# Performance work log

Measured on AMD Instinct MI355X. Metric: run time of the kernel, lower is better.

The kernel has to match this reference:

```python
import jax, jax.numpy as jnp
import numpy as np

EPS = 1e-5

def setup_inputs() -> dict:
    key = jax.random.key(0)
    ks = jax.random.split(key, 6)
    N, E, C, H, L = 50000, 800000, 128, 128, 3
    x = jax.random.normal(ks[0], (N, C), dtype=jnp.float32)
    edge_index = jax.random.randint(ks[1], (2, E), 0, N, dtype=jnp.int64)
    # Xavier-ish scaled weights; layer 0 uses in=C=H so all layers stack uniformly.
    Wl = jax.random.normal(ks[2], (L, C, H), dtype=jnp.float32) / np.sqrt(C)
    Wr = jax.random.normal(ks[3], (L, C, H), dtype=jnp.float32) / np.sqrt(C)
    b = jnp.zeros((L, H), dtype=jnp.float32)
    gamma = jnp.ones((L, H), dtype=jnp.float32)
    beta = jnp.zeros((L, H), dtype=jnp.float32)
    return {"x": x, "edge_index": edge_index, "Wl": Wl, "Wr": Wr, "b": b,
            "gamma": gamma, "beta": beta}

def _sage_bn_relu(x, src, dst, Wl, Wr, b, gamma, beta):
    N = x.shape[0]
    # mean aggregation of source features into target nodes (PyG SAGEConv default)
    agg = jax.ops.segment_sum(x[src], dst, num_segments=N)          # [N, C]
    deg = jax.ops.segment_sum(jnp.ones_like(dst, dtype=x.dtype), dst, num_segments=N)
    mean_nbr = agg / jnp.maximum(deg, 1.0)[:, None]
    h = mean_nbr @ Wl + x @ Wr + b                                   # [N, H]
    # BatchNorm1d (training-mode batch statistics over nodes)
    mu = jnp.mean(h, axis=0)
    var = jnp.var(h, axis=0)
    h = gamma * (h - mu) * jax.lax.rsqrt(var + EPS) + beta
    return jax.nn.relu(h)  # dropout omitted (deterministic reference, p->0)

def reference(x, edge_index, Wl, Wr, b, gamma, beta):
    src, dst = edge_index[0], edge_index[1]
    h = x
    for l in range(Wl.shape[0]):
        h = _sage_bn_relu(h, src, dst, Wl[l], Wr[l], b[l], gamma[l], beta[l])
    return h
```

## Files before the change

### kernel.cpp

```cpp
#include <hip/hip_runtime.h>
#include <hip/hip_bf16.h>

#define BN_EPS 1e-5f
#define BCAP 16384

typedef unsigned short u16;
typedef unsigned int u32;
typedef __attribute__((ext_vector_type(8))) short bf16x8v;
typedef __attribute__((ext_vector_type(4))) float f32x4v;

__device__ __forceinline__ float bf2f(u16 u){
    union { u32 i; float f; } c; c.i = ((u32)u) << 16; return c.f;
}
__device__ __forceinline__ u16 f2bf(float f){
    union { float f; u32 i; } c; c.f = f;
    u32 x = c.i;
    u32 r = x + 0x7FFFu + ((x >> 16) & 1u);
    return (u16)(r >> 16);
}
__device__ __forceinline__ float lo16(u32 u){
    union { u32 i; float f; } c; c.i = u << 16; return c.f;
}
__device__ __forceinline__ float hi16(u32 u){
    union { u32 i; float f; } c; c.i = u & 0xFFFF0000u; return c.f;
}
__device__ __forceinline__ u32 pack2(float f0, float f1){
    return (u32)f2bf(f0) | ((u32)f2bf(f1) << 16);
}

__global__ void detect_k(const int* __restrict__ ei, const u16* __restrict__ xu,
                         int* __restrict__ flags){
    int lane = threadIdx.x;
    unsigned long long bal = __ballot(ei[2 * lane + 1] != 0);
    int cnt = 0;
    #pragma unroll
    for (int k = 0; k < 4; ++k){
        u16 u = xu[2 * (lane + 64 * k)];
        int e = (u >> 7) & 0xFF;
        cnt += (e >= 0x70 && e <= 0x86) ? 1 : 0;
    }
    #pragma unroll
    for (int off = 1; off < 64; off <<= 1) cnt += __shfl_xor(cnt, off);
    if (lane == 0){
        flags[0] = (bal == 0ULL) ? 1 : 0;
        flags[1] = (cnt >= 128) ? 1 : 0;
    }
}

__global__ void prep_k(const void* __restrict__ x, const void* __restrict__ Wl,
                       const void* __restrict__ Wr, const void* __restrict__ b,
                       const void* __restrict__ g, const void* __restrict__ be,
                       u16* __restrict__ xb, u16* __restrict__ wT, float* __restrict__ p,
                       int total4, int wtot, int per, const int* __restrict__ flags){
    int i = blockIdx.x * blockDim.x + threadIdx.x;
    int bf = flags[1];
    if (i < total4){
        if (bf){
            ((uint2*)xb)[i] = ((const uint2*)x)[i];
        } else {
            float4 v = ((const float4*)x)[i];
            ushort4 o; o.x = f2bf(v.x); o.y = f2bf(v.y); o.z = f2bf(v.z); o.w = f2bf(v.w);
            ((ushort4*)xb)[i] = o;
        }
    }
    if (i < wtot){
        u16 vl = bf ? ((const u16*)Wl)[i] : f2bf(((const float*)Wl)[i]);
        u16 vr = bf ? ((const u16*)Wr)[i] : f2bf(((const float*)Wr)[i]);
        int l = i >> 14, r = (i >> 7) & 127, c = i & 127;
        wT[(size_t)(l * 2 + 0) * 16384 + c * 128 + r] = vl;
        wT[(size_t)(l * 2 + 1) * 16384 + c * 128 + r] = vr;
    }
    if (i < per){
        if (bf){
            p[i]           = bf2f(((const u16*)b)[i]);
            p[per + i]     = bf2f(((const u16*)g)[i]);
            p[2 * per + i] = bf2f(((const u16*)be)[i]);
        } else {
            p[i]           = ((const float*)b)[i];
            p[per + i]     = ((const float*)g)[i];
            p[2 * per + i] = ((const float*)be)[i];
        }
    }
}

__global__ __launch_bounds__(1024) void phist_k(const void* __restrict__ ei, int E,
                                                int tile, u32* __restrict__ blockHist,
                                                const int* __restrict__ flags){
    __shared__ u32 lh[128];
    int tid = threadIdx.x;
    if (tid < 128) lh[tid] = 0u;
    __syncthreads();
    int start = blockIdx.x * tile;
    int end = min(E, start + tile);
    int i64 = flags[0];
    for (int i = start + tid; i < end; i += 1024){
        int d = i64 ? (int)((const long long*)ei)[E + i] : ((const int*)ei)[E + i];
        atomicAdd(&lh[d >> 9], 1u);
    }
    __syncthreads();
    if (tid < 128) blockHist[blockIdx.x * 128 + tid] = lh[tid];
}

__global__ void bases_k(const u32* __restrict__ blockHist, u32* __restrict__ blockBase,
                        int* __restrict__ rangeBase, int* __restrict__ rowptrN, int nb){
    __shared__ u32 t_s[128];
    int k = threadIdx.x;
    u32 run = 0;
    for (int b = 0; b < nb; ++b){
        blockBase[b * 128 + k] = run;
        run += blockHist[b * 128 + k];
    }
    t_s[k] = min(run, (u32)BCAP);
    __syncthreads();
    if (k == 0){
        u32 r = 0;
        for (int j = 0; j < 128; ++j){ u32 v = t_s[j]; t_s[j] = r; r += v; }
        rangeBase[128] = (int)r;
        *rowptrN = (int)r;
    }
    __syncthreads();
    rangeBase[k] = (int)t_s[k];
}

__global__ __launch_bounds__(1024) void pscat_k(const void* __restrict__ ei, int E,
                                                int tile, const u32* __restrict__ blockBase,
                                                u32* __restrict__ part,
                                                const int* __restrict__ flags){
    __shared__ u32 lcur[128];
    int tid = threadIdx.x;
    if (tid < 128) lcur[tid] = blockBase[blockIdx.x * 128 + tid];
    __syncthreads();
    int start = blockIdx.x * tile;
    int end = min(E, start + tile);
    int i64 = flags[0];
    for (int i = start + tid; i < end; i += 1024){
        int s, d;
        if (i64){
            const long long* p = (const long long*)ei;
            s = (int)p[i]; d = (int)p[E + i];
        } else {
// ... 31 lines not shown
    #pragma unroll
    for (int off = 1; off < 64; off <<= 1){
        u32 u = __shfl_up(sc, off);
        if (lane >= off) sc += u;
    }
    if (lane == 63 && w < 8) wsum[w] = sc;
    __syncthreads();
    if (tid == 0){
        u32 r = 0;
        #pragma unroll
        for (int j = 0; j < 8; ++j){ u32 t = wsum[j]; wsum[j] = r; r += t; }
    }
    __syncthreads();
    u32 excl = (w < 8 ? wsum[w] : 0u) + sc - v;
    if (tid < 512){
        int d = d0 + tid;
        if (d < N){
            rowptr[d] = base + (int)excl;
            dinv[d] = 1.f / fmaxf((float)v, 1.f);
        }
        bins[tid] = excl;
    }
    __syncthreads();
    for (int i = tid; i < cntk; i += 1024){
        u32 e = pk[i];
        u32 pos = atomicAdd(&bins[e >> 16], 1u);
        sorted[pos] = (u16)e;
    }
    __syncthreads();
    for (int i = tid; i < cntk; i += 1024)
        col[base + i] = sorted[i];
}

__global__ void agg_k(const u16* __restrict__ h, const int* __restrict__ rowptr,
                      const u16* __restrict__ col, const float* __restrict__ dinv,
                      u16* __restrict__ meanb, int N){
    int wid  = (blockIdx.x * blockDim.x + threadIdx.x) >> 6;
    int lane = threadIdx.x & 63;
    if (wid >= N) return;
    int q   = lane >> 4;
    int sub = lane & 15;
    int s = rowptr[wid], e = rowptr[wid + 1];
    float a[8] = {0.f,0.f,0.f,0.f,0.f,0.f,0.f,0.f};
    int i = s + q;
    for (; i + 4 < e; i += 8){
        int sn0 = col[i], sn1 = col[i + 4];
        uint4 v0 = *(const uint4*)(h + (size_t)sn0 * 128 + sub * 8);
        uint4 v1 = *(const uint4*)(h + (size_t)sn1 * 128 + sub * 8);
        a[0] += lo16(v0.x) + lo16(v1.x); a[1] += hi16(v0.x) + hi16(v1.x);
        a[2] += lo16(v0.y) + lo16(v1.y); a[3] += hi16(v0.y) + hi16(v1.y);
        a[4] += lo16(v0.z) + lo16(v1.z); a[5] += hi16(v0.z) + hi16(v1.z);
        a[6] += lo16(v0.w) + lo16(v1.w); a[7] += hi16(v0.w) + hi16(v1.w);
    }
    if (i < e){
        int sn = col[i];
        uint4 v = *(const uint4*)(h + (size_t)sn * 128 + sub * 8);
        a[0] += lo16(v.x); a[1] += hi16(v.x);
        a[2] += lo16(v.y); a[3] += hi16(v.y);
        a[4] += lo16(v.z); a[5] += hi16(v.z);
        a[6] += lo16(v.w); a[7] += hi16(v.w);
    }
    #pragma unroll
    for (int off = 16; off < 64; off <<= 1){
        #pragma unroll
        for (int j = 0; j < 8; ++j) a[j] += __shfl_xor(a[j], off);
    }
    if (q == 0){
        float di = dinv[wid];
        uint4 o;
        o.x = pack2(a[0] * di, a[1] * di);
        o.y = pack2(a[2] * di, a[3] * di);
        o.z = pack2(a[4] * di, a[5] * di);
        o.w = pack2(a[6] * di, a[7] * di);
        *(uint4*)(meanb + (size_t)wid * 128 + sub * 8) = o;
    }
}

__global__ __launch_bounds__(256) void gemm_k(
        const u16* __restrict__ Aa, const u16* __restrict__ Ab,
        const u16* __restrict__ wT, const float* __restrict__ bias,
        float* __restrict__ stats, u16* __restrict__ hp16, int N, int NT){
    int tid  = threadIdx.x;
    int lane = tid & 63;
    int w    = tid >> 6;
    int hl   = lane & 15;
    int quad = lane >> 4;
    int c0   = (2 * w)     * 16 + hl;
    int c1   = (2 * w + 1) * 16 + hl;

    bf16x8v Bf[2][2][4];
    {
        const u16* bp = wT + (size_t)(2 * w) * 2048 + (size_t)hl * 128 + quad * 8;
        #pragma unroll
        for (int tl = 0; tl < 2; ++tl)
            #pragma unroll
            for (int half = 0; half < 2; ++half)
                #pragma unroll
                for (int kc = 0; kc < 4; ++kc)
                    Bf[tl][half][kc] =
                        *(const bf16x8v*)(bp + tl * 2048 + half * 16384 + kc * 32);
    }
    float bv0 = bias[c0], bv1 = bias[c1];
    float cs0 = 0.f, cq0 = 0.f, cs1 = 0.f, cq1 = 0.f;

    for (int tile = blockIdx.x; tile < NT; tile += gridDim.x){
        int m0  = tile * 32;
        int rb0 = m0;      bool v0 = (rb0 + 16 <= N); if (!v0) rb0 = N - 16;
        int rb1 = m0 + 16; bool v1 = (rb1 + 16 <= N); if (!v1) rb1 = N - 16;
        const u16* paa0 = Aa + (size_t)(rb0 + hl) * 128 + quad * 8;
        const u16* pab0 = Ab + (size_t)(rb0 + hl) * 128 + quad * 8;
        const u16* paa1 = Aa + (size_t)(rb1 + hl) * 128 + quad * 8;
        const u16* pab1 = Ab + (size_t)(rb1 + hl) * 128 + quad * 8;

        bf16x8v A0[2][4], A1[2][4];
        #pragma unroll
        for (int kc = 0; kc < 4; ++kc){
            A0[0][kc] = *(const bf16x8v*)(paa0 + kc * 32);
            A1[0][kc] = *(const bf16x8v*)(paa1 + kc * 32);
            A0[1][kc] = *(const bf16x8v*)(pab0 + kc * 32);
            A1[1][kc] = *(const bf16x8v*)(pab1 + kc * 32);
        }

        f32x4v acc0[2], acc1[2];
        #pragma unroll
        for (int tl = 0; tl < 2; ++tl){
            acc0[tl] = (f32x4v){0.f, 0.f, 0.f, 0.f};
            acc1[tl] = (f32x4v){0.f, 0.f, 0.f, 0.f};
        }
        #pragma unroll
        for (int half = 0; half < 2; ++half)
            #pragma unroll
            for (int kc = 0; kc < 4; ++kc)
                #pragma unroll
                for (int tl = 0; tl < 2; ++tl){
                    acc0[tl] = __builtin_amdgcn_mfma_f32_16x16x32_bf16(
                        A0[half][kc], Bf[tl][half][kc], acc0[tl], 0, 0, 0);
                    acc1[tl] = __builtin_amdgcn_mfma_f32_16x16x32_bf16(
                        A1[half][kc], Bf[tl][half][kc], acc1[tl], 0, 0, 0);
                }

        #pragma unroll
        for (int tl = 0; tl < 2; ++tl){
            int   c  = tl ? c1 : c0;
            float bv = tl ? bv1 : bv0;
            if (v0){
                #pragma unroll
                for (int r = 0; r < 4; ++r){
                    float v = acc0[tl][r] + bv;
                    hp16[(size_t)(rb0 + quad * 4 + r) * 128 + c] = f2bf(v);
                    if (tl){ cs1 += v; cq1 += v * v; } else { cs0 += v; cq0 += v * v; }
                }
            }
            if (v1){
                #pragma unroll
                for (int r = 0; r < 4; ++r){
                    float v = acc1[tl][r] + bv;
                    hp16[(size_t)(rb1 + quad * 4 + r) * 128 + c] = f2bf(v);
                    if (tl){ cs1 += v; cq1 += v * v; } else { cs0 += v; cq0 += v * v; }
                }
            }
        }
    }

    cs0 += __shfl_xor(cs0, 16); cs0 += __shfl_xor(cs0, 32);
    cq0 += __shfl_xor(cq0, 16); cq0 += __shfl_xor(cq0, 32);
    cs1 += __shfl_xor(cs1, 16); cs1 += __shfl_xor(cs1, 32);
    cq1 += __shfl_xor(cq1, 16); cq1 += __shfl_xor(cq1, 32);
    if (quad == 0){
        float* st = stats + (size_t)(blockIdx.x & 63) * 256;
        atomicAdd(&st[c0],       cs0);
        atomicAdd(&st[128 + c0], cq0);
        atomicAdd(&st[c1],       cs1);
        atomicAdd(&st[128 + c1], cq1);
    }
}

__global__ void finalize_k(const float* __restrict__ stats, const float* __restrict__ g,
                           const float* __restrict__ be, float* __restrict__ ss,
                           float invN){
    int j = threadIdx.x;
    float s = 0.f, sq = 0.f;
    #pragma unroll 8
    for (int bkt = 0; bkt < 64; ++bkt){
        s  += stats[bkt * 256 + j];
        sq += stats[bkt * 256 + 128 + j];
    }
    float mu  = s * invN;
    float var = sq * invN - mu * mu;
    if (!(mu == mu)) mu = 0.f;
    if (!(var >= 0.f) || !(var == var)) var = 0.f;
    float sc = g[j] * rsqrtf(var + BN_EPS);
    ss[j]       = sc;
    ss[128 + j] = be[j] - mu * sc;
}

__global__ void apply_k(const u16* __restrict__ in, const float* __restrict__ ss,
                        u16* __restrict__ outb, float* __restrict__ outf, int use_f32,
                        int total4){
    int i = blockIdx.x * blockDim.x + threadIdx.x;
    if (i >= total4) return;
    uint2 u = ((const uint2*)in)[i];
    float4 v;
    v.x = lo16(u.x); v.y = hi16(u.x); v.z = lo16(u.y); v.w = hi16(u.y);
    if (!(v.x == v.x)) v.x = 0.f;
    if (!(v.y == v.y)) v.y = 0.f;
    if (!(v.z == v.z)) v.z = 0.f;
    if (!(v.w == v.w)) v.w = 0.f;
    int c = (i & 31) * 4;
    float r0 = fmaxf(v.x * ss[c]     + ss[128 + c], 0.f);
    float r1 = fmaxf(v.y * ss[c + 1] + ss[129 + c], 0.f);
    float r2 = fmaxf(v.z * ss[c + 2] + ss[130 + c], 0.f);
    float r3 = fmaxf(v.w * ss[c + 3] + ss[131 + c], 0.f);
    if (use_f32){
        float4 o; o.x = r0; o.y = r1; o.z = r2; o.w = r3;
        ((float4*)outf)[i] = o;
    } else {
        uint2 o; o.x = pack2(r0, r1); o.y = pack2(r2, r3);
        ((uint2*)outb)[i] = o;
    }
}

extern "C" void kernel_launch(void* const* d_in, const int* in_sizes, int n_in,
                              void* d_out, int out_size, void* d_ws, size_t ws_size,
                              hipStream_t stream){
    const void* x  = d_in[0];
    const int*  ei = (const int*)d_in[1];
    const void* Wl = d_in[2];
    const void* Wr = d_in[3];
    const void* b  = d_in[4];
    const void* gm = d_in[5];
    const void* bt = d_in[6];
    float* outf = (float*)d_out;

    const int N = in_sizes[0] / 128;
    const int E = in_sizes[1] / 2;
    const int L = in_sizes[2] / 16384;
    const int PB = 128;
    const int TILE = (E + PB - 1) / PB;

    char* wsp = (char*)d_ws;
    size_t off = 0;
    auto alloc = [&](size_t bytes) -> char* {
        char* p = wsp + off;
        off = (off + bytes + 255) & ~(size_t)255;
        return p;
    };
    int*   flags  = (int*)  alloc(16);
    int*   rowptr = (int*)  alloc((size_t)(N + 1) * 4);
    u16*   col    = (u16*)  alloc((size_t)E * 2);
    float* dinv   = (float*)alloc((size_t)N * 4);
    u32*   bHist  = (u32*)  alloc((size_t)PB * 128 * 4);
    u32*   bBase  = (u32*)  alloc((size_t)PB * 128 * 4);
    int*   rangeB = (int*)  alloc((size_t)129 * 4);
    u32*   part   = (u32*)  alloc((size_t)128 * BCAP * 4);
    u16*   wT     = (u16*)  alloc((size_t)L * 2 * 16384 * 2);
    float* pvec   = (float*)alloc((size_t)3 * L * 128 * 4);
    float* ss     = (float*)alloc(256 * 4);
    float* stats  = (float*)alloc((size_t)L * 64 * 256 * 4);
    u16*   xb     = (u16*)  alloc((size_t)N * 128 * 2);
    u16*   meanb  = (u16*)  alloc((size_t)N * 128 * 2);
    u16*   hpre16 = (u16*)  alloc((size_t)N * 128 * 2);
    u16*   hA     = (u16*)  alloc((size_t)N * 128 * 2);
    u16*   hB     = (u16*)  alloc((size_t)N * 128 * 2);
    (void)ws_size; (void)n_in; (void)out_size;

    detect_k<<<1, 64, 0, stream>>>(ei, (const u16*)x, flags);
    hipMemsetAsync(stats, 0, (size_t)L * 64 * 256 * 4, stream);

    phist_k<<<PB, 1024, 0, stream>>>((const void*)ei, E, TILE, bHist, flags);
    bases_k<<<1, 128, 0, stream>>>(bHist, bBase, rangeB, rowptr + N, PB);
    pscat_k<<<PB, 1024, 0, stream>>>((const void*)ei, E, TILE, bBase, part, flags);
    build_k<<<128, 1024, 0, stream>>>(part, rangeB, rowptr, dinv, col, N);

    prep_k<<<(N * 32 + 255) / 256, 256, 0, stream>>>(x, Wl, Wr, b, gm, bt, xb, wT, pvec,
                                                     N * 32, L * 16384, L * 128, flags);

    const u16* state = xb;
    int NT      = (N + 31) / 32;
    int gblocks = (NT + 2) / 3;
    float invN  = 1.f / (float)N;
    for (int l = 0; l < L; ++l){
        int last = (l == L - 1);
        u16* nxt = (l & 1) ? hB : hA;
        agg_k<<<(N + 3) / 4, 256, 0, stream>>>(state, rowptr, col, dinv, meanb, N);
        gemm_k<<<gblocks, 256, 0, stream>>>(meanb, state, wT + (size_t)l * 2 * 16384,
                                            pvec + (size_t)l * 128,
                                            stats + (size_t)l * 64 * 256,
                                            hpre16, N, NT);
        finalize_k<<<1, 128, 0, stream>>>(stats + (size_t)l * 64 * 256,
                                          pvec + (size_t)L * 128 + l * 128,
                                          pvec + (size_t)2 * L * 128 + l * 128,
                                          ss, invN);
        apply_k<<<(N * 32 + 255) / 256, 256, 0, stream>>>(hpre16, ss, nxt, outf, last,
                                                          N * 32);
        state = nxt;
    }
}
```

Baseline: 343.2 us.

## Fold BatchNorm+ReLU into next layer's aggregation and GEMM loads

Instead of running a separate apply pass per layer, the GEMM writes pre-norm activations and the next layer's aggregation and GEMM apply the previous layer's scale/shift and ReLU on the fly as they load. The finalize kernel is folded into the GEMM through a last-block-done atomic counter that computes the next scale/shift, and only the final layer runs apply_k. This removes two launches and a full read/write of activations per layer. In exchange, agg_k redoes the normalization for every gathered neighbor (extra FMAs per edge) and the GEMM converts its A operand through bf16 again.

```diff
diff --git a/kernel.cpp b/kernel.cpp
--- a/kernel.cpp
+++ b/kernel.cpp
@@ -51,6 +51,7 @@
                        const void* __restrict__ Wr, const void* __restrict__ b,
                        const void* __restrict__ g, const void* __restrict__ be,
                        u16* __restrict__ xb, u16* __restrict__ wT, float* __restrict__ p,
+                       float* __restrict__ ssAll,
                        int total4, int wtot, int per, const int* __restrict__ flags){
     int i = blockIdx.x * blockDim.x + threadIdx.x;
     int bf = flags[1];
@@ -80,6 +81,10 @@
             p[per + i]     = ((const float*)g)[i];
             p[2 * per + i] = ((const float*)be)[i];
         }
+    }
+    if (i < 128){
+        ssAll[i]       = 1.f;
+        ssAll[128 + i] = 0.f;
     }
 }
 
@@ -205,32 +210,45 @@
 
 __global__ void agg_k(const u16* __restrict__ h, const int* __restrict__ rowptr,
                       const u16* __restrict__ col, const float* __restrict__ dinv,
-                      u16* __restrict__ meanb, int N){
+                      const float* __restrict__ ss, u16* __restrict__ meanb,
+                      float reluLo, int N){
     int wid  = (blockIdx.x * blockDim.x + threadIdx.x) >> 6;
     int lane = threadIdx.x & 63;
     if (wid >= N) return;
     int q   = lane >> 4;
     int sub = lane & 15;
+    float scr[8], shr[8];
+    #pragma unroll
+    for (int j = 0; j < 8; ++j){
+        scr[j] = ss[sub * 8 + j];
+        shr[j] = ss[128 + sub * 8 + j];
+    }
     int s = rowptr[wid], e = rowptr[wid + 1];
     float a[8] = {0.f,0.f,0.f,0.f,0.f,0.f,0.f,0.f};
     int i = s + q;
+    #define BNR(x, j) fmaxf((x) * scr[j] + shr[j], reluLo)
     for (; i + 4 < e; i += 8){
         int sn0 = col[i], sn1 = col[i + 4];
         uint4 v0 = *(const uint4*)(h + (size_t)sn0 * 128 + sub * 8);
         uint4 v1 = *(const uint4*)(h + (size_t)sn1 * 128 + sub * 8);
-        a[0] += lo16(v0.x) + lo16(v1.x); a[1] += hi16(v0.x) + hi16(v1.x);
-        a[2] += lo16(v0.y) + lo16(v1.y); a[3] += hi16(v0.y) + hi16(v1.y);
-        a[4] += lo16(v0.z) + lo16(v1.z); a[5] += hi16(v0.z) + hi16(v1.z);
-        a[6] += lo16(v0.w) + lo16(v1.w); a[7] += hi16(v0.w) + hi16(v1.w);
+        a[0] += BNR(lo16(v0.x),0) + BNR(lo16(v1.x),0);
+        a[1] += BNR(hi16(v0.x),1) + BNR(hi16(v1.x),1);
+        a[2] += BNR(lo16(v0.y),2) + BNR(lo16(v1.y),2);
+        a[3] += BNR(hi16(v0.y),3) + BNR(hi16(v1.y),3);
+        a[4] += BNR(lo16(v0.z),4) + BNR(lo16(v1.z),4);
+        a[5] += BNR(hi16(v0.z),5) + BNR(hi16(v1.z),5);
+        a[6] += BNR(lo16(v0.w),6) + BNR(lo16(v1.w),6);
+        a[7] += BNR(hi16(v0.w),7) + BNR(hi16(v1.w),7);
     }
     if (i < e){
         int sn = col[i];
         uint4 v = *(const uint4*)(h + (size_t)sn * 128 + sub * 8);
-        a[0] += lo16(v.x); a[1] += hi16(v.x);
-        a[2] += lo16(v.y); a[3] += hi16(v.y);
-        a[4] += lo16(v.z); a[5] += hi16(v.z);
-        a[6] += lo16(v.w); a[7] += hi16(v.w);
-    }
+        a[0] += BNR(lo16(v.x),0); a[1] += BNR(hi16(v.x),1);
+        a[2] += BNR(lo16(v.y),2); a[3] += BNR(hi16(v.y),3);
+        a[4] += BNR(lo16(v.z),4); a[5] += BNR(hi16(v.z),5);
+        a[6] += BNR(lo16(v.w),6); a[7] += BNR(hi16(v.w),7);
+    }
+    #undef BNR
     #pragma unroll
     for (int off = 16; off < 64; off <<= 1){
         #pragma unroll
@@ -250,7 +268,12 @@
 __global__ __launch_bounds__(256) void gemm_k(
         const u16* __restrict__ Aa, const u16* __restrict__ Ab,
         const u16* __restrict__ wT, const float* __restrict__ bias,
-        float* __restrict__ stats, u16* __restrict__ hp16, int N, int NT){
+        const float* __restrict__ ssPrev, const float* __restrict__ g,
+        const float* __restrict__ be, float* __restrict__ stats,
+        u32* __restrict__ cnt, float* __restrict__ ssNext,
+        u16* __restrict__ hOut, float reluLo, int N, int NT, float invN){
+    __shared__ float s_ss[256];
+    __shared__ u32 s_last;
     int tid  = threadIdx.x;
     int lane = tid & 63;
     int w    = tid >> 6;
@@ -258,6 +281,8 @@
     int quad = lane >> 4;
     int c0   = (2 * w)     * 16 + hl;
     int c1   = (2 * w + 1) * 16 + hl;
+    s_ss[tid] = ssPrev[tid];
+    __syncthreads();
 
     bf16x8v Bf[2][2][4];
     {
@@ -290,6 +315,18 @@
             A1[0][kc] = *(const bf16x8v*)(paa1 + kc * 32);
             A0[1][kc] = *(const bf16x8v*)(pab0 + kc * 32);
             A1[1][kc] = *(const bf16x8v*)(pab1 + kc * 32);
+        }
+        #pragma unroll
+        for (int kc = 0; kc < 4; ++kc){
+            #pragma unroll
+            for (int j = 0; j < 8; ++j){
+                int kcol = quad * 8 + kc * 32 + j;
+                float sc = s_ss[kcol], sh = s_ss[128 + kcol];
+                float f0 = fmaxf(bf2f((u16)A0[1][kc][j]) * sc + sh, reluLo);
+                float f1 = fmaxf(bf2f((u16)A1[1][kc][j]) * sc + sh, reluLo);
+                A0[1][kc][j] = (short)f2bf(f0);
+                A1[1][kc][j] = (short)f2bf(f1);
+            }
         }
 
         f32x4v acc0[2], acc1[2];
@@ -318,7 +355,7 @@
                 #pragma unroll
                 for (int r = 0; r < 4; ++r){
                     float v = acc0[tl][r] + bv;
-                    hp16[(size_t)(rb0 + quad * 4 + r) * 128 + c] = f2bf(v);
+                    hOut[(size_t)(rb0 + quad * 4 + r) * 128 + c] = f2bf(v);
                     if (tl){ cs1 += v; cq1 += v * v; } else { cs0 += v; cq0 += v * v; }
                 }
             }
@@ -326,7 +363,7 @@
                 #pragma unroll
                 for (int r = 0; r < 4; ++r){
                     float v = acc1[tl][r] + bv;
-                    hp16[(size_t)(rb1 + quad * 4 + r) * 128 + c] = f2bf(v);
+                    hOut[(size_t)(rb1 + quad * 4 + r) * 128 + c] = f2bf(v);
                     if (tl){ cs1 += v; cq1 += v * v; } else { cs0 += v; cq0 += v * v; }
                 }
             }
@@ -344,30 +381,36 @@
         atomicAdd(&st[c1],       cs1);
         atomicAdd(&st[128 + c1], cq1);
     }
-}
-
-__global__ void finalize_k(const float* __restrict__ stats, const float* __restrict__ g,
-                           const float* __restrict__ be, float* __restrict__ ss,
-                           float invN){
-    int j = threadIdx.x;
-    float s = 0.f, sq = 0.f;
-    #pragma unroll 8
-    for (int bkt = 0; bkt < 64; ++bkt){
-        s  += stats[bkt * 256 + j];
-        sq += stats[bkt * 256 + 128 + j];
-    }
-    float mu  = s * invN;
-    float var = sq * invN - mu * mu;
-    if (!(mu == mu)) mu = 0.f;
-    if (!(var >= 0.f) || !(var == var)) var = 0.f;
-    float sc = g[j] * rsqrtf(var + BN_EPS);
-    ss[j]       = sc;
-    ss[128 + j] = be[j] - mu * sc;
+    __syncthreads();
+    if (tid == 0){
+        __threadfence();
+        u32 old = __hip_atomic_fetch_add(cnt, 1u, __ATOMIC_ACQ_REL,
+                                         __HIP_MEMORY_SCOPE_AGENT);
+        s_last = (old == gridDim.x - 1) ? 1u : 0u;
+    }
+    __syncthreads();
+    if (s_last && tid < 128){
+        __threadfence();
+        float s = 0.f, sq = 0.f;
+        #pragma unroll 8
+        for (int bkt = 0; bkt < 64; ++bkt){
+            s  += __hip_atomic_load(&stats[bkt * 256 + tid],       __ATOMIC_RELAXED,
+                                    __HIP_MEMORY_SCOPE_AGENT);
+            sq += __hip_atomic_load(&stats[bkt * 256 + 128 + tid], __ATOMIC_RELAXED,
+                                    __HIP_MEMORY_SCOPE_AGENT);
+        }
+        float mu  = s * invN;
+        float var = sq * invN - mu * mu;
+        if (!(mu == mu)) mu = 0.f;
+        if (!(var >= 0.f) || !(var == var)) var = 0.f;
+        float sc = g[tid] * rsqrtf(var + BN_EPS);
+        ssNext[tid]       = sc;
+        ssNext[128 + tid] = be[tid] - mu * sc;
+    }
 }
 
 __global__ void apply_k(const u16* __restrict__ in, const float* __restrict__ ss,
-                        u16* __restrict__ outb, float* __restrict__ outf, int use_f32,
-                        int total4){
+                        float* __restrict__ outf, int total4){
     int i = blockIdx.x * blockDim.x + threadIdx.x;
     if (i >= total4) return;
     uint2 u = ((const uint2*)in)[i];
@@ -378,17 +421,12 @@
     if (!(v.z == v.z)) v.z = 0.f;
     if (!(v.w == v.w)) v.w = 0.f;
     int c = (i & 31) * 4;
-    float r0 = fmaxf(v.x * ss[c]     + ss[128 + c], 0.f);
-    float r1 = fmaxf(v.y * ss[c + 1] + ss[129 + c], 0.f);
-    float r2 = fmaxf(v.z * ss[c + 2] + ss[130 + c], 0.f);
-    float r3 = fmaxf(v.w * ss[c + 3] + ss[131 + c], 0.f);
-    if (use_f32){
-        float4 o; o.x = r0; o.y = r1; o.z = r2; o.w = r3;
-        ((float4*)outf)[i] = o;
-    } else {
-        uint2 o; o.x = pack2(r0, r1); o.y = pack2(r2, r3);
-        ((uint2*)outb)[i] = o;
-    }
+    float4 o;
+    o.x = fmaxf(v.x * ss[c]     + ss[128 + c], 0.f);
+    o.y = fmaxf(v.y * ss[c + 1] + ss[129 + c], 0.f);
+    o.z = fmaxf(v.z * ss[c + 2] + ss[130 + c], 0.f);
+    o.w = fmaxf(v.w * ss[c + 3] + ss[131 + c], 0.f);
+    ((float4*)outf)[i] = o;
 }
 
 extern "C" void kernel_launch(void* const* d_in, const int* in_sizes, int n_in,
@@ -426,17 +464,17 @@
     u32*   part   = (u32*)  alloc((size_t)128 * BCAP * 4);
     u16*   wT     = (u16*)  alloc((size_t)L * 2 * 16384 * 2);
     float* pvec   = (float*)alloc((size_t)3 * L * 128 * 4);
-    float* ss     = (float*)alloc(256 * 4);
+    float* ssAll  = (float*)alloc((size_t)(L + 1) * 256 * 4);
     float* stats  = (float*)alloc((size_t)L * 64 * 256 * 4);
+    u32*   cnt    = (u32*)  alloc((size_t)L * 256);
     u16*   xb     = (u16*)  alloc((size_t)N * 128 * 2);
     u16*   meanb  = (u16*)  alloc((size_t)N * 128 * 2);
-    u16*   hpre16 = (u16*)  alloc((size_t)N * 128 * 2);
     u16*   hA     = (u16*)  alloc((size_t)N * 128 * 2);
     u16*   hB     = (u16*)  alloc((size_t)N * 128 * 2);
     (void)ws_size; (void)n_in; (void)out_size;
 
     detect_k<<<1, 64, 0, stream>>>(ei, (const u16*)x, flags);
-    hipMemsetAsync(stats, 0, (size_t)L * 64 * 256 * 4, stream);
+    hipMemsetAsync(stats, 0, (size_t)((char*)xb - (char*)stats), stream);
 
     phist_k<<<PB, 1024, 0, stream>>>((const void*)ei, E, TILE, bHist, flags);
     bases_k<<<1, 128, 0, stream>>>(bHist, bBase, rangeB, rowptr + N, PB);
@@ -444,26 +482,29 @@
     build_k<<<128, 1024, 0, stream>>>(part, rangeB, rowptr, dinv, col, N);
 
     prep_k<<<(N * 32 + 255) / 256, 256, 0, stream>>>(x, Wl, Wr, b, gm, bt, xb, wT, pvec,
-                                                     N * 32, L * 16384, L * 128, flags);
+                                                     ssAll, N * 32, L * 16384, L * 128,
+                                                     flags);
 
     const u16* state = xb;
     int NT      = (N + 31) / 32;
     int gblocks = (NT + 2) / 3;
     float invN  = 1.f / (float)N;
     for (int l = 0; l < L; ++l){
-        int last = (l == L - 1);
         u16* nxt = (l & 1) ? hB : hA;
-        agg_k<<<(N + 3) / 4, 256, 0, stream>>>(state, rowptr, col, dinv, meanb, N);
+        float reluLo = (l == 0) ? -3.0e38f : 0.f;
+        agg_k<<<(N + 3) / 4, 256, 0, stream>>>(state, rowptr, col, dinv,
+                                               ssAll + (size_t)l * 256, meanb, reluLo, N);
         gemm_k<<<gblocks, 256, 0, stream>>>(meanb, state, wT + (size_t)l * 2 * 16384,
                                             pvec + (size_t)l * 128,
+                                            ssAll + (size_t)l * 256,
+                                            pvec + (size_t)L * 128 + (size_t)l * 128,
+                                            pvec + (size_t)2 * L * 128 + (size_t)l * 128,
                                             stats + (size_t)l * 64 * 256,
-                                            hpre16, N, NT);
-        finalize_k<<<1, 128, 0, stream>>>(stats + (size_t)l * 64 * 256,
-                                          pvec + (size_t)L * 128 + l * 128,
-                                          pvec + (size_t)2 * L * 128 + l * 128,
-                                          ss, invN);
-        apply_k<<<(N * 32 + 255) / 256, 256, 0, stream>>>(hpre16, ss, nxt, outf, last,
-                                                          N * 32);
+                                            cnt + (size_t)l * 64,
+                                            ssAll + (size_t)(l + 1) * 256,
+                                            nxt, reluLo, N, NT, invN);
         state = nxt;
     }
-}
+    apply_k<<<(N * 32 + 255) / 256, 256, 0, stream>>>(state, ssAll + (size_t)L * 256,
+                                                      outf, N * 32);
+}
```

Result: slower. 427.2 us (+24.5%).

## Double-buffer A tile loads in GEMM and fuse BN finalize into apply kernel

Applied to the files above, without the earlier changes.

The GEMM loop now prefetches the next tile's A fragments into a second register set while the current tile runs its MFMAs, with launch bounds set to two blocks per SIMD. The separate one-block finalize kernel is removed: each apply block reduces the 64 stat buckets itself, computes scale and shift in shared memory, then runs a grid-stride loop over 1024 blocks. This removes one launch per layer and hides global load latency in the GEMM, in exchange for higher register pressure and redundant stat reduction in every apply block.

```diff
diff --git a/kernel.cpp b/kernel.cpp
--- a/kernel.cpp
+++ b/kernel.cpp
@@ -247,7 +247,7 @@
     }
 }
 
-__global__ __launch_bounds__(256) void gemm_k(
+__global__ __launch_bounds__(256, 2) void gemm_k(
         const u16* __restrict__ Aa, const u16* __restrict__ Ab,
         const u16* __restrict__ wT, const float* __restrict__ bias,
         float* __restrict__ stats, u16* __restrict__ hp16, int N, int NT){
@@ -274,64 +274,84 @@
     float bv0 = bias[c0], bv1 = bias[c1];
     float cs0 = 0.f, cq0 = 0.f, cs1 = 0.f, cq1 = 0.f;
 
-    for (int tile = blockIdx.x; tile < NT; tile += gridDim.x){
-        int m0  = tile * 32;
-        int rb0 = m0;      bool v0 = (rb0 + 16 <= N); if (!v0) rb0 = N - 16;
-        int rb1 = m0 + 16; bool v1 = (rb1 + 16 <= N); if (!v1) rb1 = N - 16;
-        const u16* paa0 = Aa + (size_t)(rb0 + hl) * 128 + quad * 8;
-        const u16* pab0 = Ab + (size_t)(rb0 + hl) * 128 + quad * 8;
-        const u16* paa1 = Aa + (size_t)(rb1 + hl) * 128 + quad * 8;
-        const u16* pab1 = Ab + (size_t)(rb1 + hl) * 128 + quad * 8;
-
-        bf16x8v A0[2][4], A1[2][4];
-        #pragma unroll
-        for (int kc = 0; kc < 4; ++kc){
-            A0[0][kc] = *(const bf16x8v*)(paa0 + kc * 32);
-            A1[0][kc] = *(const bf16x8v*)(paa1 + kc * 32);
-            A0[1][kc] = *(const bf16x8v*)(pab0 + kc * 32);
-            A1[1][kc] = *(const bf16x8v*)(pab1 + kc * 32);
-        }
-
-        f32x4v acc0[2], acc1[2];
-        #pragma unroll
-        for (int tl = 0; tl < 2; ++tl){
-            acc0[tl] = (f32x4v){0.f, 0.f, 0.f, 0.f};
-            acc1[tl] = (f32x4v){0.f, 0.f, 0.f, 0.f};
-        }
-        #pragma unroll
-        for (int half = 0; half < 2; ++half)
-            #pragma unroll
-            for (int kc = 0; kc < 4; ++kc)
-                #pragma unroll
-                for (int tl = 0; tl < 2; ++tl){
-                    acc0[tl] = __builtin_amdgcn_mfma_f32_16x16x32_bf16(
-                        A0[half][kc], Bf[tl][half][kc], acc0[tl], 0, 0, 0);
-                    acc1[tl] = __builtin_amdgcn_mfma_f32_16x16x32_bf16(
-                        A1[half][kc], Bf[tl][half][kc], acc1[tl], 0, 0, 0);
-                }
-
-        #pragma unroll
-        for (int tl = 0; tl < 2; ++tl){
-            int   c  = tl ? c1 : c0;
-            float bv = tl ? bv1 : bv0;
-            if (v0){
-                #pragma unroll
-                for (int r = 0; r < 4; ++r){
-                    float v = acc0[tl][r] + bv;
-                    hp16[(size_t)(rb0 + quad * 4 + r) * 128 + c] = f2bf(v);
-                    if (tl){ cs1 += v; cq1 += v * v; } else { cs0 += v; cq0 += v * v; }
-                }
-            }
-            if (v1){
-                #pragma unroll
-                for (int r = 0; r < 4; ++r){
-                    float v = acc1[tl][r] + bv;
-                    hp16[(size_t)(rb1 + quad * 4 + r) * 128 + c] = f2bf(v);
-                    if (tl){ cs1 += v; cq1 += v * v; } else { cs0 += v; cq0 += v * v; }
-                }
-            }
-        }
-    }
+    size_t laneoff = (size_t)hl * 128 + quad * 8;
+    bf16x8v AX[2][2][4], AY[2][2][4];
+
+#define LOADA(DST, T) { \
+    int m0_ = (T) * 32; \
+    int rb0_ = m0_;      if (rb0_ + 16 > N) rb0_ = N - 16; \
+    int rb1_ = m0_ + 16; if (rb1_ + 16 > N) rb1_ = N - 16; \
+    const u16* pa0_ = Aa + (size_t)rb0_ * 128 + laneoff; \
+    const u16* pb0_ = Ab + (size_t)rb0_ * 128 + laneoff; \
+    const u16* pa1_ = Aa + (size_t)rb1_ * 128 + laneoff; \
+    const u16* pb1_ = Ab + (size_t)rb1_ * 128 + laneoff; \
+    _Pragma("unroll") \
+    for (int kc_ = 0; kc_ < 4; ++kc_){ \
+        DST[0][0][kc_] = *(const bf16x8v*)(pa0_ + kc_ * 32); \
+        DST[1][0][kc_] = *(const bf16x8v*)(pa1_ + kc_ * 32); \
+        DST[0][1][kc_] = *(const bf16x8v*)(pb0_ + kc_ * 32); \
+        DST[1][1][kc_] = *(const bf16x8v*)(pb1_ + kc_ * 32); \
+    } }
+
+#define PROC(SRC, T) { \
+    int m0_ = (T) * 32; \
+    int rb0_ = m0_;      bool v0_ = (m0_ + 16 <= N); if (!v0_) rb0_ = N - 16; \
+    int rb1_ = m0_ + 16; bool v1_ = (m0_ + 32 <= N); if (!v1_) rb1_ = N - 16; \
+    f32x4v acc0_[2], acc1_[2]; \
+    acc0_[0] = (f32x4v){0.f,0.f,0.f,0.f}; acc0_[1] = (f32x4v){0.f,0.f,0.f,0.f}; \
+    acc1_[0] = (f32x4v){0.f,0.f,0.f,0.f}; acc1_[1] = (f32x4v){0.f,0.f,0.f,0.f}; \
+    _Pragma("unroll") \
+    for (int half_ = 0; half_ < 2; ++half_) \
+        _Pragma("unroll") \
+        for (int kc_ = 0; kc_ < 4; ++kc_) \
+            _Pragma("unroll") \
+            for (int tl_ = 0; tl_ < 2; ++tl_){ \
+                acc0_[tl_] = __builtin_amdgcn_mfma_f32_16x16x32_bf16( \
+                    SRC[0][half_][kc_], Bf[tl_][half_][kc_], acc0_[tl_], 0, 0, 0); \
+                acc1_[tl_] = __builtin_amdgcn_mfma_f32_16x16x32_bf16( \
+                    SRC[1][half_][kc_], Bf[tl_][half_][kc_], acc1_[tl_], 0, 0, 0); \
+            } \
+    _Pragma("unroll") \
+    for (int tl_ = 0; tl_ < 2; ++tl_){ \
+        int   c_  = tl_ ? c1 : c0; \
+        float bv_ = tl_ ? bv1 : bv0; \
+        if (v0_){ \
+            _Pragma("unroll") \
+            for (int r_ = 0; r_ < 4; ++r_){ \
+                float vv_ = acc0_[tl_][r_] + bv_; \
+                hp16[(size_t)(rb0_ + quad * 4 + r_) * 128 + c_] = f2bf(vv_); \
+                if (tl_){ cs1 += vv_; cq1 += vv_ * vv_; } else { cs0 += vv_; cq0 += vv_ * vv_; } \
+            } \
+        } \
+        if (v1_){ \
+            _Pragma("unroll") \
+            for (int r_ = 0; r_ < 4; ++r_){ \
+                float vv_ = acc1_[tl_][r_] + bv_; \
+                hp16[(size_t)(rb1_ + quad * 4 + r_) * 128 + c_] = f2bf(vv_); \
+                if (tl_){ cs1 += vv_; cq1 += vv_ * vv_; } else { cs0 += vv_; cq0 += vv_ * vv_; } \
+            } \
+        } \
+    } }
+
+    int t = blockIdx.x;
+    int G = gridDim.x;
+    if (t < NT){
+        LOADA(AX, t);
+        for (;;){
+            int tn = t + G;
+            if (tn < NT) LOADA(AY, tn);
+            PROC(AX, t);
+            t = tn;
+            if (t >= NT) break;
+            tn = t + G;
+            if (tn < NT) LOADA(AX, tn);
+            PROC(AY, t);
+            t = tn;
+            if (t >= NT) break;
+        }
+    }
+#undef LOADA
+#undef PROC
 
     cs0 += __shfl_xor(cs0, 16); cs0 += __shfl_xor(cs0, 32);
     cq0 += __shfl_xor(cq0, 16); cq0 += __shfl_xor(cq0, 32);
@@ -346,48 +366,53 @@
     }
 }
 
-__global__ void finalize_k(const float* __restrict__ stats, const float* __restrict__ g,
-                           const float* __restrict__ be, float* __restrict__ ss,
-                           float invN){
-    int j = threadIdx.x;
-    float s = 0.f, sq = 0.f;
+__global__ __launch_bounds__(256) void apply_k(
+        const u16* __restrict__ in, const float* __restrict__ stats,
+        const float* __restrict__ g, const float* __restrict__ be,
+        u16* __restrict__ outb, float* __restrict__ outf, int use_f32,
+        int total4, float invN){
+    __shared__ float s_red[256];
+    __shared__ float s_ss[256];
+    int tid = threadIdx.x;
+    float s = 0.f;
     #pragma unroll 8
-    for (int bkt = 0; bkt < 64; ++bkt){
-        s  += stats[bkt * 256 + j];
-        sq += stats[bkt * 256 + 128 + j];
-    }
-    float mu  = s * invN;
-    float var = sq * invN - mu * mu;
-    if (!(mu == mu)) mu = 0.f;
-    if (!(var >= 0.f) || !(var == var)) var = 0.f;
-    float sc = g[j] * rsqrtf(var + BN_EPS);
-    ss[j]       = sc;
-    ss[128 + j] = be[j] - mu * sc;
-}
-
-__global__ void apply_k(const u16* __restrict__ in, const float* __restrict__ ss,
-                        u16* __restrict__ outb, float* __restrict__ outf, int use_f32,
-                        int total4){
-    int i = blockIdx.x * blockDim.x + threadIdx.x;
-    if (i >= total4) return;
-    uint2 u = ((const uint2*)in)[i];
-    float4 v;
-    v.x = lo16(u.x); v.y = hi16(u.x); v.z = lo16(u.y); v.w = hi16(u.y);
-    if (!(v.x == v.x)) v.x = 0.f;
-    if (!(v.y == v.y)) v.y = 0.f;
-    if (!(v.z == v.z)) v.z = 0.f;
-    if (!(v.w == v.w)) v.w = 0.f;
-    int c = (i & 31) * 4;
-    float r0 = fmaxf(v.x * ss[c]     + ss[128 + c], 0.f);
-    float r1 = fmaxf(v.y * ss[c + 1] + ss[129 + c], 0.f);
-    float r2 = fmaxf(v.z * ss[c + 2] + ss[130 + c], 0.f);
-    float r3 = fmaxf(v.w * ss[c + 3] + ss[131 + c], 0.f);
-    if (use_f32){
-        float4 o; o.x = r0; o.y = r1; o.z = r2; o.w = r3;
-        ((float4*)outf)[i] = o;
-    } else {
-        uint2 o; o.x = pack2(r0, r1); o.y = pack2(r2, r3);
-        ((uint2*)outb)[i] = o;
+    for (int bkt = 0; bkt < 64; ++bkt) s += stats[bkt * 256 + tid];
+    s_red[tid] = s;
+    __syncthreads();
+    if (tid < 128){
+        float mu  = s_red[tid] * invN;
+        float var = s_red[128 + tid] * invN - mu * mu;
+        if (!(mu == mu)) mu = 0.f;
+        if (!(var >= 0.f) || !(var == var)) var = 0.f;
+        float sc = g[tid] * rsqrtf(var + BN_EPS);
+        s_ss[tid]       = sc;
+        s_ss[128 + tid] = be[tid] - mu * sc;
+    }
+    __syncthreads();
+    int c = (tid & 31) * 4;
+    float sc0 = s_ss[c],     sh0 = s_ss[128 + c];
+    float sc1 = s_ss[c + 1], sh1 = s_ss[129 + c];
+    float sc2 = s_ss[c + 2], sh2 = s_ss[130 + c];
+    float sc3 = s_ss[c + 3], sh3 = s_ss[131 + c];
+    for (int i = blockIdx.x * blockDim.x + tid; i < total4; i += blockDim.x * gridDim.x){
+        uint2 u = ((const uint2*)in)[i];
+        float4 v;
+        v.x = lo16(u.x); v.y = hi16(u.x); v.z = lo16(u.y); v.w = hi16(u.y);
+        if (!(v.x == v.x)) v.x = 0.f;
+        if (!(v.y == v.y)) v.y = 0.f;
+        if (!(v.z == v.z)) v.z = 0.f;
+        if (!(v.w == v.w)) v.w = 0.f;
+        float r0 = fmaxf(v.x * sc0 + sh0, 0.f);
+        float r1 = fmaxf(v.y * sc1 + sh1, 0.f);
+        float r2 = fmaxf(v.z * sc2 + sh2, 0.f);
+        float r3 = fmaxf(v.w * sc3 + sh3, 0.f);
+        if (use_f32){
+            float4 o; o.x = r0; o.y = r1; o.z = r2; o.w = r3;
+            ((float4*)outf)[i] = o;
+        } else {
+            uint2 o; o.x = pack2(r0, r1); o.y = pack2(r2, r3);
+            ((uint2*)outb)[i] = o;
+        }
     }
 }
 
@@ -426,7 +451,6 @@
     u32*   part   = (u32*)  alloc((size_t)128 * BCAP * 4);
     u16*   wT     = (u16*)  alloc((size_t)L * 2 * 16384 * 2);
     float* pvec   = (float*)alloc((size_t)3 * L * 128 * 4);
-    float* ss     = (float*)alloc(256 * 4);
     float* stats  = (float*)alloc((size_t)L * 64 * 256 * 4);
     u16*   xb     = (u16*)  alloc((size_t)N * 128 * 2);
     u16*   meanb  = (u16*)  alloc((size_t)N * 128 * 2);
@@ -458,12 +482,10 @@
                                             pvec + (size_t)l * 128,
                                             stats + (size_t)l * 64 * 256,
                                             hpre16, N, NT);
-        finalize_k<<<1, 128, 0, stream>>>(stats + (size_t)l * 64 * 256,
+        apply_k<<<1024, 256, 0, stream>>>(hpre16, stats + (size_t)l * 64 * 256,
                                           pvec + (size_t)L * 128 + l * 128,
                                           pvec + (size_t)2 * L * 128 + l * 128,
-                                          ss, invN);
-        apply_k<<<(N * 32 + 255) / 256, 256, 0, stream>>>(hpre16, ss, nxt, outf, last,
-                                                          N * 32);
+                                          nxt, outf, last, N * 32, invN);
         state = nxt;
     }
 }
```

Result: no change. 339.7 us (-1.0%).

## Fuse neighbor aggregation into GEMM via shared memory and merge BN finalize into apply

Applied to the files above, without the earlier changes.

Neighbor mean aggregation now runs inside the GEMM kernel. Each block gathers neighbor rows for its 32-node tile into shared memory and feeds them straight to MFMA, so the meanb intermediate buffer and a separate launch go away. The BN finalize kernel is folded into the apply kernel: every block recomputes the scale and shift from the per-bucket stats, and apply becomes grid-stride over 1024 blocks. The risk is that the gather now runs with only about 560 blocks of 256 threads and 8 rows per wave serialized, which may expose gather latency that the old high-occupancy agg_k hid.

```diff
diff --git a/kernel.cpp b/kernel.cpp
--- a/kernel.cpp
+++ b/kernel.cpp
@@ -106,6 +106,7 @@
     __shared__ u32 t_s[128];
     int k = threadIdx.x;
     u32 run = 0;
+    #pragma unroll 8
     for (int b = 0; b < nb; ++b){
         blockBase[b * 128 + k] = run;
         run += blockHist[b * 128 + k];
@@ -203,54 +204,12 @@
         col[base + i] = sorted[i];
 }
 
-__global__ void agg_k(const u16* __restrict__ h, const int* __restrict__ rowptr,
-                      const u16* __restrict__ col, const float* __restrict__ dinv,
-                      u16* __restrict__ meanb, int N){
-    int wid  = (blockIdx.x * blockDim.x + threadIdx.x) >> 6;
-    int lane = threadIdx.x & 63;
-    if (wid >= N) return;
-    int q   = lane >> 4;
-    int sub = lane & 15;
-    int s = rowptr[wid], e = rowptr[wid + 1];
-    float a[8] = {0.f,0.f,0.f,0.f,0.f,0.f,0.f,0.f};
-    int i = s + q;
-    for (; i + 4 < e; i += 8){
-        int sn0 = col[i], sn1 = col[i + 4];
-        uint4 v0 = *(const uint4*)(h + (size_t)sn0 * 128 + sub * 8);
-        uint4 v1 = *(const uint4*)(h + (size_t)sn1 * 128 + sub * 8);
-        a[0] += lo16(v0.x) + lo16(v1.x); a[1] += hi16(v0.x) + hi16(v1.x);
-        a[2] += lo16(v0.y) + lo16(v1.y); a[3] += hi16(v0.y) + hi16(v1.y);
-        a[4] += lo16(v0.z) + lo16(v1.z); a[5] += hi16(v0.z) + hi16(v1.z);
-        a[6] += lo16(v0.w) + lo16(v1.w); a[7] += hi16(v0.w) + hi16(v1.w);
-    }
-    if (i < e){
-        int sn = col[i];
-        uint4 v = *(const uint4*)(h + (size_t)sn * 128 + sub * 8);
-        a[0] += lo16(v.x); a[1] += hi16(v.x);
-        a[2] += lo16(v.y); a[3] += hi16(v.y);
-        a[4] += lo16(v.z); a[5] += hi16(v.z);
-        a[6] += lo16(v.w); a[7] += hi16(v.w);
-    }
-    #pragma unroll
-    for (int off = 16; off < 64; off <<= 1){
-        #pragma unroll
-        for (int j = 0; j < 8; ++j) a[j] += __shfl_xor(a[j], off);
-    }
-    if (q == 0){
-        float di = dinv[wid];
-        uint4 o;
-        o.x = pack2(a[0] * di, a[1] * di);
-        o.y = pack2(a[2] * di, a[3] * di);
-        o.z = pack2(a[4] * di, a[5] * di);
-        o.w = pack2(a[6] * di, a[7] * di);
-        *(uint4*)(meanb + (size_t)wid * 128 + sub * 8) = o;
-    }
-}
-
-__global__ __launch_bounds__(256) void gemm_k(
-        const u16* __restrict__ Aa, const u16* __restrict__ Ab,
+__global__ __launch_bounds__(256, 2) void agemm_k(
+        const u16* __restrict__ state, const int* __restrict__ rowptr,
+        const u16* __restrict__ col, const float* __restrict__ dinv,
         const u16* __restrict__ wT, const float* __restrict__ bias,
         float* __restrict__ stats, u16* __restrict__ hp16, int N, int NT){
+    __shared__ __align__(16) u16 s_mean[32][136];
     int tid  = threadIdx.x;
     int lane = tid & 63;
     int w    = tid >> 6;
@@ -274,60 +233,130 @@
     float bv0 = bias[c0], bv1 = bias[c1];
     float cs0 = 0.f, cq0 = 0.f, cs1 = 0.f, cq1 = 0.f;
 
-    for (int tile = blockIdx.x; tile < NT; tile += gridDim.x){
-        int m0  = tile * 32;
-        int rb0 = m0;      bool v0 = (rb0 + 16 <= N); if (!v0) rb0 = N - 16;
-        int rb1 = m0 + 16; bool v1 = (rb1 + 16 <= N); if (!v1) rb1 = N - 16;
-        const u16* paa0 = Aa + (size_t)(rb0 + hl) * 128 + quad * 8;
-        const u16* pab0 = Ab + (size_t)(rb0 + hl) * 128 + quad * 8;
-        const u16* paa1 = Aa + (size_t)(rb1 + hl) * 128 + quad * 8;
-        const u16* pab1 = Ab + (size_t)(rb1 + hl) * 128 + quad * 8;
-
-        bf16x8v A0[2][4], A1[2][4];
+    int G = gridDim.x;
+    for (int t = blockIdx.x; t < NT; t += G){
+        int m0  = t * 32;
+        int rb0 = m0;      bool tv0 = (m0 + 16 <= N); if (!tv0) rb0 = N - 16;
+        int rb1 = m0 + 16; bool tv1 = (m0 + 32 <= N); if (!tv1) rb1 = N - 16;
+
+        const u16* p1a = state + (size_t)(rb0 + hl) * 128 + quad * 8;
+        const u16* p1b = state + (size_t)(rb1 + hl) * 128 + quad * 8;
+        bf16x8v A1a[4], A1b[4];
         #pragma unroll
         for (int kc = 0; kc < 4; ++kc){
-            A0[0][kc] = *(const bf16x8v*)(paa0 + kc * 32);
-            A1[0][kc] = *(const bf16x8v*)(paa1 + kc * 32);
-            A0[1][kc] = *(const bf16x8v*)(pab0 + kc * 32);
-            A1[1][kc] = *(const bf16x8v*)(pab1 + kc * 32);
-        }
+            A1a[kc] = *(const bf16x8v*)(p1a + kc * 32);
+            A1b[kc] = *(const bf16x8v*)(p1b + kc * 32);
+        }
+
+        #pragma unroll 1
+        for (int d8 = 0; d8 < 8; ++d8){
+            int row = w * 8 + d8;
+            int wid = m0 + row;
+            if (wid < N){
+                int s = rowptr[wid], e = rowptr[wid + 1];
+                float a[8] = {0.f,0.f,0.f,0.f,0.f,0.f,0.f,0.f};
+                int i = s + quad;
+                for (; i + 12 < e; i += 16){
+                    int sn0 = col[i], sn1 = col[i + 4], sn2 = col[i + 8], sn3 = col[i + 12];
+                    uint4 g0 = *(const uint4*)(state + (size_t)sn0 * 128 + hl * 8);
+                    uint4 g1 = *(const uint4*)(state + (size_t)sn1 * 128 + hl * 8);
+                    uint4 g2 = *(const uint4*)(state + (size_t)sn2 * 128 + hl * 8);
+                    uint4 g3 = *(const uint4*)(state + (size_t)sn3 * 128 + hl * 8);
+                    a[0] += lo16(g0.x) + lo16(g1.x) + lo16(g2.x) + lo16(g3.x);
+                    a[1] += hi16(g0.x) + hi16(g1.x) + hi16(g2.x) + hi16(g3.x);
+                    a[2] += lo16(g0.y) + lo16(g1.y) + lo16(g2.y) + lo16(g3.y);
+                    a[3] += hi16(g0.y) + hi16(g1.y) + hi16(g2.y) + hi16(g3.y);
+                    a[4] += lo16(g0.z) + lo16(g1.z) + lo16(g2.z) + lo16(g3.z);
+                    a[5] += hi16(g0.z) + hi16(g1.z) + hi16(g2.z) + hi16(g3.z);
+                    a[6] += lo16(g0.w) + lo16(g1.w) + lo16(g2.w) + lo16(g3.w);
+                    a[7] += hi16(g0.w) + hi16(g1.w) + hi16(g2.w) + hi16(g3.w);
+                }
+                for (; i + 4 < e; i += 8){
+                    int sn0 = col[i], sn1 = col[i + 4];
+                    uint4 g0 = *(const uint4*)(state + (size_t)sn0 * 128 + hl * 8);
+                    uint4 g1 = *(const uint4*)(state + (size_t)sn1 * 128 + hl * 8);
+                    a[0] += lo16(g0.x) + lo16(g1.x); a[1] += hi16(g0.x) + hi16(g1.x);
+                    a[2] += lo16(g0.y) + lo16(g1.y); a[3] += hi16(g0.y) + hi16(g1.y);
+                    a[4] += lo16(g0.z) + lo16(g1.z); a[5] += hi16(g0.z) + hi16(g1.z);
+                    a[6] += lo16(g0.w) + lo16(g1.w); a[7] += hi16(g0.w) + hi16(g1.w);
+                }
+                if (i < e){
+                    int sn = col[i];
+                    uint4 g0 = *(const uint4*)(state + (size_t)sn * 128 + hl * 8);
+                    a[0] += lo16(g0.x); a[1] += hi16(g0.x);
+                    a[2] += lo16(g0.y); a[3] += hi16(g0.y);
+                    a[4] += lo16(g0.z); a[5] += hi16(g0.z);
+                    a[6] += lo16(g0.w); a[7] += hi16(g0.w);
+                }
+                #pragma unroll
+                for (int off = 16; off < 64; off <<= 1){
+                    #pragma unroll
+                    for (int j = 0; j < 8; ++j) a[j] += __shfl_xor(a[j], off);
+                }
+                if (quad == 0){
+                    float di = dinv[wid];
+                    uint4 o;
+                    o.x = pack2(a[0] * di, a[1] * di);
+                    o.y = pack2(a[2] * di, a[3] * di);
+                    o.z = pack2(a[4] * di, a[5] * di);
+                    o.w = pack2(a[6] * di, a[7] * di);
+                    *(uint4*)(&s_mean[row][hl * 8]) = o;
+                }
+            } else if (quad == 0){
+                uint4 z; z.x = 0u; z.y = 0u; z.z = 0u; z.w = 0u;
+                *(uint4*)(&s_mean[row][hl * 8]) = z;
+            }
+        }
+        __syncthreads();
+
+        bf16x8v A0a[4], A0b[4];
+        #pragma unroll
+        for (int kc = 0; kc < 4; ++kc){
+            A0a[kc] = *(const bf16x8v*)(&s_mean[hl][quad * 8 + kc * 32]);
+            A0b[kc] = *(const bf16x8v*)(&s_mean[16 + hl][quad * 8 + kc * 32]);
+        }
+        __syncthreads();
 
         f32x4v acc0[2], acc1[2];
-        #pragma unroll
-        for (int tl = 0; tl < 2; ++tl){
-            acc0[tl] = (f32x4v){0.f, 0.f, 0.f, 0.f};
-            acc1[tl] = (f32x4v){0.f, 0.f, 0.f, 0.f};
-        }
-        #pragma unroll
-        for (int half = 0; half < 2; ++half)
+        acc0[0] = (f32x4v){0.f,0.f,0.f,0.f}; acc0[1] = (f32x4v){0.f,0.f,0.f,0.f};
+        acc1[0] = (f32x4v){0.f,0.f,0.f,0.f}; acc1[1] = (f32x4v){0.f,0.f,0.f,0.f};
+        #pragma unroll
+        for (int kc = 0; kc < 4; ++kc)
             #pragma unroll
-            for (int kc = 0; kc < 4; ++kc)
-                #pragma unroll
-                for (int tl = 0; tl < 2; ++tl){
-                    acc0[tl] = __builtin_amdgcn_mfma_f32_16x16x32_bf16(
-                        A0[half][kc], Bf[tl][half][kc], acc0[tl], 0, 0, 0);
-                    acc1[tl] = __builtin_amdgcn_mfma_f32_16x16x32_bf16(
-                        A1[half][kc], Bf[tl][half][kc], acc1[tl], 0, 0, 0);
-                }
+            for (int tl = 0; tl < 2; ++tl){
+                acc0[tl] = __builtin_amdgcn_mfma_f32_16x16x32_bf16(
+                    A0a[kc], Bf[tl][0][kc], acc0[tl], 0, 0, 0);
+                acc1[tl] = __builtin_amdgcn_mfma_f32_16x16x32_bf16(
+                    A0b[kc], Bf[tl][0][kc], acc1[tl], 0, 0, 0);
+            }
+        #pragma unroll
+        for (int kc = 0; kc < 4; ++kc)
+            #pragma unroll
+            for (int tl = 0; tl < 2; ++tl){
+                acc0[tl] = __builtin_amdgcn_mfma_f32_16x16x32_bf16(
+                    A1a[kc], Bf[tl][1][kc], acc0[tl], 0, 0, 0);
+                acc1[tl] = __builtin_amdgcn_mfma_f32_16x16x32_bf16(
+                    A1b[kc], Bf[tl][1][kc], acc1[tl], 0, 0, 0);
+            }
 
         #pragma unroll
         for (int tl = 0; tl < 2; ++tl){
             int   c  = tl ? c1 : c0;
             float bv = tl ? bv1 : bv0;
-            if (v0){
+            if (tv0){
                 #pragma unroll
                 for (int r = 0; r < 4; ++r){
-                    float v = acc0[tl][r] + bv;
-                    hp16[(size_t)(rb0 + quad * 4 + r) * 128 + c] = f2bf(v);
-                    if (tl){ cs1 += v; cq1 += v * v; } else { cs0 += v; cq0 += v * v; }
+                    float vv = acc0[tl][r] + bv;
+                    hp16[(size_t)(rb0 + quad * 4 + r) * 128 + c] = f2bf(vv);
+                    if (tl){ cs1 += vv; cq1 += vv * vv; } else { cs0 += vv; cq0 += vv * vv; }
                 }
             }
-            if (v1){
+            if (tv1){
                 #pragma unroll
                 for (int r = 0; r < 4; ++r){
-                    float v = acc1[tl][r] + bv;
-                    hp16[(size_t)(rb1 + quad * 4 + r) * 128 + c] = f2bf(v);
-                    if (tl){ cs1 += v; cq1 += v * v; } else { cs0 += v; cq0 += v * v; }
+                    float vv = acc1[tl][r] + bv;
+                    hp16[(size_t)(rb1 + quad * 4 + r) * 128 + c] = f2bf(vv);
+                    if (tl){ cs1 += vv; cq1 += vv * vv; } else { cs0 += vv; cq0 += vv * vv; }
                 }
             }
         }
@@ -346,48 +375,53 @@
     }
 }
 
-__global__ void finalize_k(const float* __restrict__ stats, const float* __restrict__ g,
-                           const float* __restrict__ be, float* __restrict__ ss,
-                           float invN){
-    int j = threadIdx.x;
-    float s = 0.f, sq = 0.f;
+__global__ __launch_bounds__(256) void apply_k(
+        const u16* __restrict__ in, const float* __restrict__ stats,
+        const float* __restrict__ g, const float* __restrict__ be,
+        u16* __restrict__ outb, float* __restrict__ outf, int use_f32,
+        int total4, float invN){
+    __shared__ float s_red[256];
+    __shared__ float s_ss[256];
+    int tid = threadIdx.x;
+    float s = 0.f;
     #pragma unroll 8
-    for (int bkt = 0; bkt < 64; ++bkt){
-        s  += stats[bkt * 256 + j];
-        sq += stats[bkt * 256 + 128 + j];
-    }
-    float mu  = s * invN;
-    float var = sq * invN - mu * mu;
-    if (!(mu == mu)) mu = 0.f;
-    if (!(var >= 0.f) || !(var == var)) var = 0.f;
-    float sc = g[j] * rsqrtf(var + BN_EPS);
-    ss[j]       = sc;
-    ss[128 + j] = be[j] - mu * sc;
-}
-
-__global__ void apply_k(const u16* __restrict__ in, const float* __restrict__ ss,
-                        u16* __restrict__ outb, float* __restrict__ outf, int use_f32,
-                        int total4){
-    int i = blockIdx.x * blockDim.x + threadIdx.x;
-    if (i >= total4) return;
-    uint2 u = ((const uint2*)in)[i];
-    float4 v;
-    v.x = lo16(u.x); v.y = hi16(u.x); v.z = lo16(u.y); v.w = hi16(u.y);
-    if (!(v.x == v.x)) v.x = 0.f;
-    if (!(v.y == v.y)) v.y = 0.f;
-    if (!(v.z == v.z)) v.z = 0.f;
-    if (!(v.w == v.w)) v.w = 0.f;
-    int c = (i & 31) * 4;
-    float r0 = fmaxf(v.x * ss[c]     + ss[128 + c], 0.f);
-    float r1 = fmaxf(v.y * ss[c + 1] + ss[129 + c], 0.f);
-    float r2 = fmaxf(v.z * ss[c + 2] + ss[130 + c], 0.f);
-    float r3 = fmaxf(v.w * ss[c + 3] + ss[131 + c], 0.f);
-    if (use_f32){
-        float4 o; o.x = r0; o.y = r1; o.z = r2; o.w = r3;
-        ((float4*)outf)[i] = o;
-    } else {
-        uint2 o; o.x = pack2(r0, r1); o.y = pack2(r2, r3);
-        ((uint2*)outb)[i] = o;
+    for (int bkt = 0; bkt < 64; ++bkt) s += stats[bkt * 256 + tid];
+    s_red[tid] = s;
+    __syncthreads();
+    if (tid < 128){
+        float mu  = s_red[tid] * invN;
+        float var = s_red[128 + tid] * invN - mu * mu;
+        if (!(mu == mu)) mu = 0.f;
+        if (!(var >= 0.f) || !(var == var)) var = 0.f;
+        float sc = g[tid] * rsqrtf(var + BN_EPS);
+        s_ss[tid]       = sc;
+        s_ss[128 + tid] = be[tid] - mu * sc;
+    }
+    __syncthreads();
+    int c = (tid & 31) * 4;
+    float sc0 = s_ss[c],     sh0 = s_ss[128 + c];
+    float sc1 = s_ss[c + 1], sh1 = s_ss[129 + c];
+    float sc2 = s_ss[c + 2], sh2 = s_ss[130 + c];
+    float sc3 = s_ss[c + 3], sh3 = s_ss[131 + c];
+    for (int i = blockIdx.x * blockDim.x + tid; i < total4; i += blockDim.x * gridDim.x){
+        uint2 u = ((const uint2*)in)[i];
+        float4 v;
+        v.x = lo16(u.x); v.y = hi16(u.x); v.z = lo16(u.y); v.w = hi16(u.y);
+        if (!(v.x == v.x)) v.x = 0.f;
+        if (!(v.y == v.y)) v.y = 0.f;
+        if (!(v.z == v.z)) v.z = 0.f;
+        if (!(v.w == v.w)) v.w = 0.f;
+        float r0 = fmaxf(v.x * sc0 + sh0, 0.f);
+        float r1 = fmaxf(v.y * sc1 + sh1, 0.f);
+        float r2 = fmaxf(v.z * sc2 + sh2, 0.f);
+        float r3 = fmaxf(v.w * sc3 + sh3, 0.f);
+        if (use_f32){
+            float4 o; o.x = r0; o.y = r1; o.z = r2; o.w = r3;
+            ((float4*)outf)[i] = o;
+        } else {
+            uint2 o; o.x = pack2(r0, r1); o.y = pack2(r2, r3);
+            ((uint2*)outb)[i] = o;
+        }
     }
 }
 
@@ -426,10 +460,8 @@
     u32*   part   = (u32*)  alloc((size_t)128 * BCAP * 4);
     u16*   wT     = (u16*)  alloc((size_t)L * 2 * 16384 * 2);
     float* pvec   = (float*)alloc((size_t)3 * L * 128 * 4);
-    float* ss     = (float*)alloc(256 * 4);
     float* stats  = (float*)alloc((size_t)L * 64 * 256 * 4);
     u16*   xb     = (u16*)  alloc((size_t)N * 128 * 2);
-    u16*   meanb  = (u16*)  alloc((size_t)N * 128 * 2);
     u16*   hpre16 = (u16*)  alloc((size_t)N * 128 * 2);
     u16*   hA     = (u16*)  alloc((size_t)N * 128 * 2);
     u16*   hB     = (u16*)  alloc((size_t)N * 128 * 2);
@@ -453,17 +485,15 @@
     for (int l = 0; l < L; ++l){
         int last = (l == L - 1);
         u16* nxt = (l & 1) ? hB : hA;
-        agg_k<<<(N + 3) / 4, 256, 0, stream>>>(state, rowptr, col, dinv, meanb, N);
-        gemm_k<<<gblocks, 256, 0, stream>>>(meanb, state, wT + (size_t)l * 2 * 16384,
-                                            pvec + (size_t)l * 128,
-                                            stats + (size_t)l * 64 * 256,
-                                            hpre16, N, NT);
-        finalize_k<<<1, 128, 0, stream>>>(stats + (size_t)l * 64 * 256,
+        agemm_k<<<gblocks, 256, 0, stream>>>(state, rowptr, col, dinv,
+                                             wT + (size_t)l * 2 * 16384,
+                                             pvec + (size_t)l * 128,
+                                             stats + (size_t)l * 64 * 256,
+                                             hpre16, N, NT);
+        apply_k<<<1024, 256, 0, stream>>>(hpre16, stats + (size_t)l * 64 * 256,
                                           pvec + (size_t)L * 128 + l * 128,
                                           pvec + (size_t)2 * L * 128 + l * 128,
-                                          ss, invN);
-        apply_k<<<(N * 32 + 255) / 256, 256, 0, stream>>>(hpre16, ss, nxt, outf, last,
-                                                          N * 32);
+                                          nxt, outf, last, N * 32, invN);
         state = nxt;
     }
 }
```

After: 521.1 us. +51.9%, slower.
